# Kernel optimization log

Hardware: AMD Instinct MI355X
Metric: run time of the kernel (lower is better)

## Reference

```python
import jax, jax.numpy as jnp
import numpy as np


def _quant(x):
    # Per-tensor dynamic uint8 quantization to produce LUT row/col indices.
    # (The CUDA kernel's exact requant scheme is not in the source; this is the
    # assumed scheme: scale so max |x| -> 255, round, clip to [0,255].)
    s = 255.0 / jnp.maximum(jnp.max(jnp.abs(x)), jnp.float32(1e-6))
    return jnp.clip(jnp.round(x * s), 0, 255).astype(jnp.int32)


def _lut_conv(x, w, b, lut):
    # CustomAnyConv2d: stride=1, padding=(2,2), kernel 5x5.
    O, Cin, kh, kw = w.shape
    # im2col patches: (B, Cin*kh*kw, H, W), feature ordering matches w.reshape(O, -1)
    patches = jax.lax.conv_general_dilated_patches(
        x, (kh, kw), (1, 1), ((2, 2), (2, 2)))
    B, K, H, W = patches.shape
    pi = _quant(patches).reshape(B, K, H * W)            # (B,K,P)
    wi = _quant(w.reshape(O, K))                          # (O,K)
    vals = lut[pi[:, None, :, :], wi[None, :, :, None]]   # (B,O,K,P) gather
    out = vals.sum(axis=2).reshape(B, O, H, W)            # accumulate LUT products
    return out + b[None, :, None, None]


def _lut_dense(x, w, b, lut):
    # CustomAnyDense: out[h, o] = sum_k LUT[x[h,k], w[o,k]] + b[o]
    xi = _quant(x)                                        # (B,K)
    wi = _quant(w)                                        # (O,K)
    vals = lut[xi[:, None, :], wi[None, :, :]]            # (B,O,K)
    return vals.sum(axis=2) + b


def _maxpool2(x, pad=0):
    return jax.lax.reduce_window(
        x, -jnp.inf, jax.lax.max,
        (1, 1, 2, 2), (1, 1, 2, 2),
        ((0, 0), (0, 0), (pad, pad), (pad, pad)))


def setup_inputs() -> dict:
    key = jax.random.key(0)
    ks = jax.random.split(key, 11)
    B = 32
    x = jax.random.uniform(ks[0], (B, 1, 28, 28), jnp.float32)
    ij = np.arange(256)
    # Approximate-multiplier LUT: high byte of exact 8x8-bit product (uint8-valued).
    lut = jnp.asarray(((ij[:, None] * ij[None, :]) >> 8).astype(np.float32))
    return {
        "x": x,
        "lut": lut,
        "w1": jax.random.uniform(ks[1], (16, 1, 5, 5), jnp.float32),
        "b1": jax.random.normal(ks[2], (16,), jnp.float32) * 0.01,
        "w2": jax.random.uniform(ks[3], (32, 16, 5, 5), jnp.float32),
        "b2": jax.random.normal(ks[4], (32,), jnp.float32) * 0.01,
        "w3": jax.random.uniform(ks[5], (64, 32, 5, 5), jnp.float32),
        "b3": jax.random.normal(ks[6], (64,), jnp.float32) * 0.01,
        "fw1": jax.random.uniform(ks[7], (256, 1024), jnp.float32),
        "fb1": jax.random.normal(ks[8], (256,), jnp.float32) * 0.01,
        "fw2": jax.random.uniform(ks[9], (10, 256), jnp.float32),
        "fb2": jax.random.normal(ks[10], (10,), jnp.float32) * 0.01,
    }


def reference(x, lut, w1, b1, w2, b2, w3, b3, fw1, fb1, fw2, fb2):
    h = jax.nn.relu(_lut_conv(x, w1, b1, lut))
    h = _maxpool2(h)                     # (B,16,14,14)
    h = jax.nn.relu(_lut_conv(h, w2, b2, lut))
    h = _maxpool2(h)                     # (B,32,7,7)
    h = jax.nn.relu(_lut_conv(h, w3, b3, lut))
    h = _maxpool2(h, pad=1)              # (B,64,4,4)
    h = h.reshape(h.shape[0], -1)        # (B,1024)
    h = jax.nn.relu(_lut_dense(h, fw1, fb1, lut))
    h = _lut_dense(h, fw2, fb2, lut)     # (B,10)
    return jax.nn.log_softmax(h, axis=1)
```

## Files before the change

kernel.cpp:

```cpp
#include <hip/hip_runtime.h>
#include <math.h>

typedef unsigned int  u32;
typedef unsigned short u16;
typedef unsigned short u16x2 __attribute__((ext_vector_type(2)));

#define MAGIC 0x5A17D0E5u

#define O_FLAGS 256
#define O_QFW1  4096
#define O_QFW2  528384
#define O_A1    533504
#define O_A2    934912
#define O_A3    1135616
#define O_A4    1266688

__device__ __forceinline__ float blk_max(float v, float* red) {
  int t = threadIdx.x;
  __syncthreads();
  red[t] = v;
  __syncthreads();
#pragma unroll
  for (int s = 128; s > 0; s >>= 1) {
    if (t < s) red[t] = fmaxf(red[t], red[t + s]);
    __syncthreads();
  }
  return red[0];
}

__device__ __forceinline__ void amax_f(float* slot, float v) {
  atomicMax((int*)slot, (int)__float_as_uint(v));
}

__device__ __forceinline__ u16 quant1(float v, float s) {
  float q = rintf(v * s);
  q = fminf(fmaxf(q, 0.0f), 255.0f);
  return (u16)q;
}

__device__ __forceinline__ void mac_u32(u32& acc, u32 a, u32 w) {
  u16x2 av = __builtin_bit_cast(u16x2, a);
  u16x2 wv = __builtin_bit_cast(u16x2, w);
  u16x2 p  = av * wv;
  acc += (__builtin_bit_cast(u32, p) >> 8) & 0x00FF00FFu;
}
__device__ __forceinline__ void mac4(u32& acc, uint4 a, uint4 w) {
  mac_u32(acc, a.x, w.x); mac_u32(acc, a.y, w.y);
  mac_u32(acc, a.z, w.z); mac_u32(acc, a.w, w.w);
}

__device__ __forceinline__ float fmax4(float4 v) {
  return fmaxf(fmaxf(fabsf(v.x), fabsf(v.y)), fmaxf(fabsf(v.z), fabsf(v.w)));
}

__global__ __launch_bounds__(256) void k_conv1(
    const float* __restrict__ x, const float* __restrict__ w1, const float* __restrict__ b1,
    const float* __restrict__ w2, const float* __restrict__ w3,
    const float* __restrict__ fw1, const float* __restrict__ fw2,
    float* __restrict__ a1, float* wsf) {
  __shared__ unsigned char sx[32 * 32];
  __shared__ u16 sw[32];
  __shared__ float red[256];
  const int t = threadIdx.x, bid = blockIdx.x;

  if (bid >= 512) {
    int sb = bid - 512;
    const float* p; int n4, base, nb, slot;
    if (sb < 2)       { p = w2;  n4 = 3200;  base = sb;      nb = 2;  slot = 2; }
    else if (sb < 10) { p = w3;  n4 = 12800; base = sb - 2;  nb = 8;  slot = 3; }
    else if (sb < 58) { p = fw1; n4 = 65536; base = sb - 10; nb = 48; slot = 4; }
    else              { p = fw2; n4 = 640;   base = 0;       nb = 1;  slot = 5; }
    const float4* p4 = (const float4*)p;
    float m = 0.f;
    for (int i = base * 256 + t; i < n4; i += nb * 256) m = fmaxf(m, fmax4(p4[i]));
    m = blk_max(m, red);
    if (t == 0) amax_f(wsf + slot, m);
    return;
  }

  int b = bid >> 4, oc = bid & 15;
  float m = 0.f;
  const float4* x4 = (const float4*)x;
  for (int i = t; i < 6272; i += 256) m = fmaxf(m, fmax4(x4[i]));
  float xmax = blk_max(m, red);
  m = 0.f;
  if (t < 100) m = fmax4(((const float4*)w1)[t]);
  float w1max = blk_max(m, red);
  float s0 = 255.0f / fmaxf(xmax, 1e-6f);
  float sw1 = 255.0f / fmaxf(w1max, 1e-6f);

  u32* sxz = (u32*)sx;
  for (int i = t; i < 256; i += 256) sxz[i] = 0;
  __syncthreads();
  for (int i = t; i < 784; i += 256) {
    int y = i / 28, xx = i - y * 28;
    sx[(y + 2) * 32 + xx + 2] = (unsigned char)quant1(x[b * 784 + i], s0);
  }
  if (t < 25) sw[t] = quant1(w1[oc * 25 + t], sw1);
  __syncthreads();
  float lm = 0.f;
  if (t < 196) {
    int py = t / 14, px = t - py * 14;
    int best = -2147483647;
#pragma unroll
    for (int dy = 0; dy < 2; ++dy)
#pragma unroll
      for (int dx = 0; dx < 2; ++dx) {
        int cy = 2 * py + dy, cx = 2 * px + dx;
        int acc = 0;
#pragma unroll
        for (int kh = 0; kh < 5; ++kh) {
          const unsigned char* xp = sx + (cy + kh) * 32 + cx;
#pragma unroll
          for (int kw = 0; kw < 5; ++kw)
            acc += ((int)xp[kw] * (int)sw[kh * 5 + kw]) >> 8;
        }
        best = max(best, acc);
      }
    float v = fmaxf(0.f, (float)best + b1[oc]);
    a1[b * 3136 + t * 16 + oc] = v;
    lm = v;
  }
  lm = blk_max(lm, red);
  if (t == 0) amax_f(wsf + 6, lm);
}

__global__ __launch_bounds__(256) void k_conv2(
    const float* __restrict__ a1, const float* __restrict__ w2, const float* __restrict__ b2,
    const float* __restrict__ fw1, const float* __restrict__ fw2,
    float* __restrict__ a2, u16* __restrict__ qfw1, u16* __restrict__ qfw2, float* wsf) {
  __shared__ __align__(16) u16 sa[324 * 16];
  __shared__ __align__(16) u16 sw[800];
  __shared__ int sconv[196];
  __shared__ float red[256];
  const int t = threadIdx.x, bid = blockIdx.x;

  if (bid >= 512) {
    if (bid < 576) {
      float s = 255.0f / fmaxf(wsf[4], 1e-6f);
      for (int i = (bid - 512) * 256 + t; i < 262144; i += 64 * 256)
        qfw1[i] = quant1(fw1[i], s);
    } else {
      float s = 255.0f / fmaxf(wsf[5], 1e-6f);
      for (int i = t; i < 2560; i += 256) qfw2[i] = quant1(fw2[i], s);
    }
    return;
  }

  int b = bid >> 4, og = bid & 15;
  float s1 = 255.0f / fmaxf(wsf[6], 1e-6f);
  float sw2 = 255.0f / fmaxf(wsf[2], 1e-6f);
  u32* sz = (u32*)sa;
  for (int i = t; i < 2592; i += 256) sz[i] = 0;
  __syncthreads();
  for (int i = t; i < 3136; i += 256) {
    int px = i >> 4, c = i & 15;
    int y = px / 14, xx = px - y * 14;
    sa[((y + 2) * 18 + xx + 2) * 16 + c] = quant1(a1[b * 3136 + i], s1);
  }
  for (int i = t; i < 800; i += 256) {
    int ol = i / 400, r = i - ol * 400, c = r / 25, tp = r - c * 25;
    sw[ol * 400 + tp * 16 + c] = quant1(w2[(og * 2 + ol) * 400 + c * 25 + tp], sw2);
  }
  __syncthreads();
  int h = t & 1, pxb = t >> 1;
  float lm = 0.f;
  for (int ol = 0; ol < 2; ++ol) {
    int oc = og * 2 + ol;
    const uint4* wq = (const uint4*)(sw + ol * 400);
#pragma unroll
    for (int rep = 0; rep < 2; ++rep) {
      int px = pxb + rep * 128;
      if (px < 196) {
        int y = px / 14, xx = px - y * 14;
        u32 acc = 0;
#pragma unroll
        for (int kh = 0; kh < 5; ++kh)
#pragma unroll
          for (int kw = 0; kw < 5; ++kw) {
            int row = (y + kh) * 18 + (xx + kw);
            uint4 av = *(const uint4*)(sa + row * 16 + h * 8);
            mac4(acc, av, wq[(kh * 5 + kw) * 2 + h]);
          }
        int ai = (int)((acc & 0xFFFFu) + (acc >> 16));
        ai += __shfl_down(ai, 1, 2);
        if (h == 0) sconv[px] = ai;
      }
    }
    __syncthreads();
    if (t < 49) {
      int py = t / 7, px = t - py * 7;
      int mm = sconv[(2 * py) * 14 + 2 * px];
      mm = max(mm, sconv[(2 * py) * 14 + 2 * px + 1]);
      mm = max(mm, sconv[(2 * py + 1) * 14 + 2 * px]);
      mm = max(mm, sconv[(2 * py + 1) * 14 + 2 * px + 1]);
      float v = fmaxf(0.f, (float)mm + b2[oc]);
      a2[b * 1568 + t * 32 + oc] = v;
      lm = fmaxf(lm, v);
    }
    __syncthreads();
  }
  lm = blk_max(lm, red);
  if (t == 0) amax_f(wsf + 7, lm);
}

__global__ __launch_bounds__(256) void k_conv3(
    const float* __restrict__ a2, const float* __restrict__ w3, const float* __restrict__ b3,
    float* __restrict__ a3, float* wsf) {
  __shared__ __align__(16) u16 sa[121 * 40];
  __shared__ __align__(16) u16 sw[4 * 800];
  __shared__ float red[256];
  const int t = threadIdx.x, bid = blockIdx.x;
  int b = bid >> 4, og = bid & 15;
  float s2 = 255.0f / fmaxf(wsf[7], 1e-6f);
  float sw3 = 255.0f / fmaxf(wsf[3], 1e-6f);
  u32* sz = (u32*)sa;
  for (int i = t; i < 2420; i += 256) sz[i] = 0;
  __syncthreads();
  for (int i = t; i < 1568; i += 256) {
    int px = i >> 5, c = i & 31;
    int y = px / 7, xx = px - y * 7;
    sa[((y + 2) * 11 + xx + 2) * 40 + c] = quant1(a2[b * 1568 + i], s2);
  }
  for (int i = t; i < 3200; i += 256) {
    int ol = i / 800, r = i - ol * 800, c = r / 25, tp = r - c * 25;
    sw[ol * 800 + tp * 32 + c] = quant1(w3[(og * 4 + ol) * 800 + c * 25 + tp], sw3);
  }
  __syncthreads();
  int q = t & 3, pos = t >> 2;
  int dydx = pos & 3, r = pos >> 2;
  int py = r >> 2, px = r & 3;
  int cy = 2 * py - 1 + (dydx >> 1), cx = 2 * px - 1 + (dydx & 1);
  bool valid = (cy >= 0 && cy < 7 && cx >= 0 && cx < 7);
  float lm = 0.f;
  for (int ol = 0; ol < 4; ++ol) {
    int oc = og * 4 + ol;
    int ai = 0;
    if (valid) {
      u32 acc = 0;
#pragma unroll
      for (int kh = 0; kh < 5; ++kh)
#pragma unroll
        for (int kw = 0; kw < 5; ++kw) {
          int row = (cy + kh) * 11 + (cx + kw);
          uint4 av = *(const uint4*)(sa + row * 40 + q * 8);
          uint4 wv = *(const uint4*)(sw + ol * 800 + (kh * 5 + kw) * 32 + q * 8);
          mac4(acc, av, wv);
        }
      ai = (int)((acc & 0xFFFFu) + (acc >> 16));
    }
    ai += __shfl_down(ai, 2, 4);
    ai += __shfl_down(ai, 1, 4);
    int val = valid ? ai : -(1 << 30);
    int mm = max(val, __shfl_down(val, 4, 16));
    mm = max(mm, __shfl_down(mm, 8, 16));
    if ((t & 15) == 0) {
      float v = fmaxf(0.f, (float)mm + b3[oc]);
      a3[b * 1024 + oc * 16 + r] = v;
      lm = fmaxf(lm, v);
    }
  }
  lm = blk_max(lm, red);
  if (t == 0) amax_f(wsf + 8, lm);
}

__global__ __launch_bounds__(256) void k_dense12(
    const float* __restrict__ a3f, const u16* __restrict__ qfw1, const float* __restrict__ fb1,
    const u16* __restrict__ qfw2, const float* __restrict__ fb2,
    float* __restrict__ a4, float* __restrict__ out, float* wsf, u32* flags) {
  __shared__ union {
    struct { u16 sh[1024]; } p;
    struct { u16 sh2[32 * 264]; float zb[320]; } w;
  } sm;
  __shared__ float red[256];
  const int t = threadIdx.x, bid = blockIdx.x;

  if (bid < 512) {
    int b = bid >> 4, og = bid & 15;
    float s3 = 255.0f / fmaxf(wsf[8], 1e-6f);
    for (int i = t; i < 1024; i += 256)
      sm.p.sh[i] = quant1(a3f[b * 1024 + i], s3);
    __syncthreads();
    int ol = t >> 4, ks = t & 15;
    int o = og * 16 + ol;
    const uint4* wp = (const uint4*)(qfw1 + o * 1024);
    const uint4* hp = (const uint4*)sm.p.sh;
    u32 acc = 0;
#pragma unroll
    for (int j = 0; j < 8; ++j)
      mac4(acc, hp[j * 16 + ks], wp[j * 16 + ks]);
    int ai = (int)((acc & 0xFFFFu) + (acc >> 16));
#pragma unroll
    for (int d = 8; d > 0; d >>= 1)
      ai += __shfl_down(ai, d, 16);
    float lm = 0.f;
    if (ks == 0) {
      float v = fmaxf(0.f, (float)ai + fb1[o]);
      a4[b * 256 + o] = v;
      lm = v;
    }
    lm = blk_max(lm, red);
    if (t == 0) amax_f(wsf + 9, lm);
    __syncthreads();
    if (t == 0)
      __hip_atomic_store(&flags[bid], MAGIC, __ATOMIC_RELEASE, __HIP_MEMORY_SCOPE_AGENT);
    return;
  }

  {
    long it = 0;
    int ok = 0;
    do {
      u32 f1 = __hip_atomic_load(&flags[t],       __ATOMIC_RELAXED, __HIP_MEMORY_SCOPE_AGENT);
      u32 f2 = __hip_atomic_load(&flags[t + 256], __ATOMIC_RELAXED, __HIP_MEMORY_SCOPE_AGENT);
      ok = __syncthreads_and((f1 == MAGIC) && (f2 == MAGIC));
      if (!ok) __builtin_amdgcn_s_sleep(1);
    } while (!ok && ++it < 4000000);
    __threadfence();
  }
  float s4 = 255.0f / fmaxf(wsf[9], 1e-6f);
  for (int i = t; i < 8192; i += 256) {
    int b = i >> 8, k = i & 255;
    sm.w.sh2[b * 264 + k] = quant1(a4[i], s4);
  }
  __syncthreads();
  for (int task = t; task < 320; task += 256) {
    int b = task / 10, o = task - b * 10;
    const uint4* wp = (const uint4*)(qfw2 + o * 256);
    const uint4* hp = (const uint4*)(sm.w.sh2 + b * 264);
    u32 acc = 0;
#pragma unroll
    for (int j = 0; j < 32; ++j)
      mac4(acc, hp[j], wp[j]);
    sm.w.zb[task] = (float)((acc & 0xFFFFu) + (acc >> 16)) + fb2[o];
  }
  __syncthreads();
  for (int task = t; task < 320; task += 256) {
    int b = task / 10;
    const float* z = sm.w.zb + b * 10;
    float m = z[0];
#pragma unroll
    for (int j = 1; j < 10; ++j) m = fmaxf(m, z[j]);
    float se = 0.f;
#pragma unroll
    for (int j = 0; j < 10; ++j) se += expf(z[j] - m);
    out[task] = sm.w.zb[task] - (m + logf(se));
  }
}

extern "C" void kernel_launch(void* const* d_in, const int* in_sizes, int n_in,
                              void* d_out, int out_size, void* d_ws, size_t ws_size,
                              hipStream_t stream) {
  const float* x   = (const float*)d_in[0];
  const float* w1  = (const float*)d_in[2];
  const float* b1  = (const float*)d_in[3];
  const float* w2  = (const float*)d_in[4];
  const float* b2  = (const float*)d_in[5];
  const float* w3  = (const float*)d_in[6];
  const float* b3  = (const float*)d_in[7];
  const float* fw1 = (const float*)d_in[8];
  const float* fb1 = (const float*)d_in[9];
  const float* fw2 = (const float*)d_in[10];
  const float* fb2 = (const float*)d_in[11];
  float* out = (float*)d_out;
  unsigned char* ws8 = (unsigned char*)d_ws;
  float* wsf = (float*)d_ws;
  u32* flags = (u32*)(ws8 + O_FLAGS);
  u16* QFW1 = (u16*)(ws8 + O_QFW1);
  u16* QFW2 = (u16*)(ws8 + O_QFW2);
  float* A1 = (float*)(ws8 + O_A1);
  float* A2 = (float*)(ws8 + O_A2);
  float* A3 = (float*)(ws8 + O_A3);
  float* A4 = (float*)(ws8 + O_A4);

  k_conv1  <<<571, 256, 0, stream>>>(x, w1, b1, w2, w3, fw1, fw2, A1, wsf);
  k_conv2  <<<577, 256, 0, stream>>>(A1, w2, b2, fw1, fw2, A2, QFW1, QFW2, wsf);
  k_conv3  <<<512, 256, 0, stream>>>(A2, w3, b3, A3, wsf);
  k_dense12<<<513, 256, 0, stream>>>(A3, QFW1, fb1, QFW2, fb2, A4, out, wsf, flags);
}
```

Measured before the change: 148.3 us.

## Split x-max into flag-signalled blocks, fuse fw1/fw2 quantization into dense kernel

```diff
diff --git a/kernel.cpp b/kernel.cpp
--- a/kernel.cpp
+++ b/kernel.cpp
@@ -7,13 +7,12 @@
 
 #define MAGIC 0x5A17D0E5u
 
-#define O_FLAGS 256
-#define O_QFW1  4096
-#define O_QFW2  528384
-#define O_A1    533504
-#define O_A2    934912
-#define O_A3    1135616
-#define O_A4    1266688
+#define O_XFLAGS 256
+#define O_FLAGS  1024
+#define O_A1     4096
+#define O_A2     405504
+#define O_A3     606208
+#define O_A4     737280
 
 __device__ __forceinline__ float blk_max(float v, float* red) {
   int t = threadIdx.x;
@@ -53,18 +52,31 @@
   return fmaxf(fmaxf(fabsf(v.x), fabsf(v.y)), fmaxf(fabsf(v.z), fabsf(v.w)));
 }
 
-__global__ __launch_bounds__(256) void k_conv1(
+__global__ __launch_bounds__(256, 2) void k_conv1(
     const float* __restrict__ x, const float* __restrict__ w1, const float* __restrict__ b1,
     const float* __restrict__ w2, const float* __restrict__ w3,
     const float* __restrict__ fw1, const float* __restrict__ fw2,
-    float* __restrict__ a1, float* wsf) {
-  __shared__ unsigned char sx[32 * 32];
-  __shared__ u16 sw[32];
+    float* __restrict__ a1, float* wsf, u32* xflags) {
+  __shared__ float sxf[1024];
+  __shared__ unsigned char sx[1024];
+  __shared__ u16 sw[64];
   __shared__ float red[256];
   const int t = threadIdx.x, bid = blockIdx.x;
 
-  if (bid >= 512) {
-    int sb = bid - 512;
+  if (bid >= 256) {
+    int sb = bid - 256;
+    if (sb < 16) {
+      const float4* x4 = (const float4*)x;
+      float m = 0.f;
+      for (int i = sb * 256 + t; i < 6272; i += 16 * 256) m = fmaxf(m, fmax4(x4[i]));
+      m = blk_max(m, red);
+      if (t == 0) {
+        amax_f(wsf + 0, m);
+        __hip_atomic_store(&xflags[sb], MAGIC, __ATOMIC_RELEASE, __HIP_MEMORY_SCOPE_AGENT);
+      }
+      return;
+    }
+    sb -= 16;
     const float* p; int n4, base, nb, slot;
     if (sb < 2)       { p = w2;  n4 = 3200;  base = sb;      nb = 2;  slot = 2; }
     else if (sb < 10) { p = w3;  n4 = 12800; base = sb - 2;  nb = 8;  slot = 3; }
@@ -78,48 +90,57 @@
     return;
   }
 
-  int b = bid >> 4, oc = bid & 15;
+  int b = bid >> 3, op = bid & 7;
   float m = 0.f;
-  const float4* x4 = (const float4*)x;
-  for (int i = t; i < 6272; i += 256) m = fmaxf(m, fmax4(x4[i]));
-  float xmax = blk_max(m, red);
-  m = 0.f;
   if (t < 100) m = fmax4(((const float4*)w1)[t]);
   float w1max = blk_max(m, red);
-  float s0 = 255.0f / fmaxf(xmax, 1e-6f);
-  float sw1 = 255.0f / fmaxf(w1max, 1e-6f);
-
-  u32* sxz = (u32*)sx;
-  for (int i = t; i < 256; i += 256) sxz[i] = 0;
+  float sw1s = 255.0f / fmaxf(w1max, 1e-6f);
+  for (int i = t; i < 1024; i += 256) sxf[i] = 0.f;
   __syncthreads();
   for (int i = t; i < 784; i += 256) {
     int y = i / 28, xx = i - y * 28;
-    sx[(y + 2) * 32 + xx + 2] = (unsigned char)quant1(x[b * 784 + i], s0);
-  }
-  if (t < 25) sw[t] = quant1(w1[oc * 25 + t], sw1);
+    sxf[(y + 2) * 32 + xx + 2] = x[b * 784 + i];
+  }
+  if (t < 50) sw[t] = quant1(w1[op * 50 + t], sw1s);
+  {
+    int it = 0, ok = 0;
+    do {
+      u32 f = (t < 16) ? __hip_atomic_load(&xflags[t], __ATOMIC_RELAXED, __HIP_MEMORY_SCOPE_AGENT)
+                       : MAGIC;
+      ok = __syncthreads_and(f == MAGIC);
+      if (!ok) __builtin_amdgcn_s_sleep(1);
+    } while (!ok && ++it < 2000000);
+    __threadfence();
+  }
+  float s0 = 255.0f / fmaxf(wsf[0], 1e-6f);
+  for (int i = t; i < 1024; i += 256) sx[i] = (unsigned char)quant1(sxf[i], s0);
   __syncthreads();
   float lm = 0.f;
   if (t < 196) {
     int py = t / 14, px = t - py * 14;
-    int best = -2147483647;
-#pragma unroll
-    for (int dy = 0; dy < 2; ++dy)
-#pragma unroll
-      for (int dx = 0; dx < 2; ++dx) {
-        int cy = 2 * py + dy, cx = 2 * px + dx;
-        int acc = 0;
-#pragma unroll
-        for (int kh = 0; kh < 5; ++kh) {
-          const unsigned char* xp = sx + (cy + kh) * 32 + cx;
-#pragma unroll
-          for (int kw = 0; kw < 5; ++kw)
-            acc += ((int)xp[kw] * (int)sw[kh * 5 + kw]) >> 8;
+#pragma unroll
+    for (int ol = 0; ol < 2; ++ol) {
+      int oc = op * 2 + ol;
+      int best = -2147483647;
+#pragma unroll
+      for (int dy = 0; dy < 2; ++dy)
+#pragma unroll
+        for (int dx = 0; dx < 2; ++dx) {
+          int cy = 2 * py + dy, cx = 2 * px + dx;
+          int acc = 0;
+#pragma unroll
+          for (int kh = 0; kh < 5; ++kh) {
+            const unsigned char* xp = sx + (cy + kh) * 32 + cx;
+#pragma unroll
+            for (int kw = 0; kw < 5; ++kw)
+              acc += ((int)xp[kw] * (int)sw[ol * 25 + kh * 5 + kw]) >> 8;
+          }
+          best = max(best, acc);
         }
-        best = max(best, acc);
-      }
-    float v = fmaxf(0.f, (float)best + b1[oc]);
-    a1[b * 3136 + t * 16 + oc] = v;
-    lm = v;
+      float v = fmaxf(0.f, (float)best + b1[oc]);
+      a1[b * 3136 + t * 16 + oc] = v;
+      lm = fmaxf(lm, v);
+    }
   }
   lm = blk_max(lm, red);
   if (t == 0) amax_f(wsf + 6, lm);
@@ -127,26 +148,12 @@
 
 __global__ __launch_bounds__(256) void k_conv2(
     const float* __restrict__ a1, const float* __restrict__ w2, const float* __restrict__ b2,
-    const float* __restrict__ fw1, const float* __restrict__ fw2,
-    float* __restrict__ a2, u16* __restrict__ qfw1, u16* __restrict__ qfw2, float* wsf) {
+    float* __restrict__ a2, float* wsf) {
   __shared__ __align__(16) u16 sa[324 * 16];
   __shared__ __align__(16) u16 sw[800];
   __shared__ int sconv[196];
   __shared__ float red[256];
   const int t = threadIdx.x, bid = blockIdx.x;
-
-  if (bid >= 512) {
-    if (bid < 576) {
-      float s = 255.0f / fmaxf(wsf[4], 1e-6f);
-      for (int i = (bid - 512) * 256 + t; i < 262144; i += 64 * 256)
-        qfw1[i] = quant1(fw1[i], s);
-    } else {
-      float s = 255.0f / fmaxf(wsf[5], 1e-6f);
-      for (int i = t; i < 2560; i += 256) qfw2[i] = quant1(fw2[i], s);
-    }
-    return;
-  }
-
   int b = bid >> 4, og = bid & 15;
   float s1 = 255.0f / fmaxf(wsf[6], 1e-6f);
   float sw2 = 255.0f / fmaxf(wsf[2], 1e-6f);
@@ -265,12 +272,12 @@
 }
 
 __global__ __launch_bounds__(256) void k_dense12(
-    const float* __restrict__ a3f, const u16* __restrict__ qfw1, const float* __restrict__ fb1,
-    const u16* __restrict__ qfw2, const float* __restrict__ fb2,
+    const float* __restrict__ a3f, const float* __restrict__ fw1, const float* __restrict__ fb1,
+    const float* __restrict__ fw2, const float* __restrict__ fb2,
     float* __restrict__ a4, float* __restrict__ out, float* wsf, u32* flags) {
   __shared__ union {
     struct { u16 sh[1024]; } p;
-    struct { u16 sh2[32 * 264]; float zb[320]; } w;
+    struct { u16 sh2[32 * 264]; u16 qw[2560]; float zb[320]; } w;
   } sm;
   __shared__ float red[256];
   const int t = threadIdx.x, bid = blockIdx.x;
@@ -278,17 +285,26 @@
   if (bid < 512) {
     int b = bid >> 4, og = bid & 15;
     float s3 = 255.0f / fmaxf(wsf[8], 1e-6f);
+    float sws = 255.0f / fmaxf(wsf[4], 1e-6f);
     for (int i = t; i < 1024; i += 256)
       sm.p.sh[i] = quant1(a3f[b * 1024 + i], s3);
     __syncthreads();
     int ol = t >> 4, ks = t & 15;
     int o = og * 16 + ol;
-    const uint4* wp = (const uint4*)(qfw1 + o * 1024);
+    const float4* wf = (const float4*)(fw1 + o * 1024);
     const uint4* hp = (const uint4*)sm.p.sh;
     u32 acc = 0;
 #pragma unroll
-    for (int j = 0; j < 8; ++j)
-      mac4(acc, hp[j * 16 + ks], wp[j * 16 + ks]);
+    for (int j = 0; j < 8; ++j) {
+      int e = j * 16 + ks;
+      float4 f0 = wf[e * 2], f1 = wf[e * 2 + 1];
+      uint4 wv;
+      wv.x = (u32)quant1(f0.x, sws) | ((u32)quant1(f0.y, sws) << 16);
+      wv.y = (u32)quant1(f0.z, sws) | ((u32)quant1(f0.w, sws) << 16);
+      wv.z = (u32)quant1(f1.x, sws) | ((u32)quant1(f1.y, sws) << 16);
+      wv.w = (u32)quant1(f1.z, sws) | ((u32)quant1(f1.w, sws) << 16);
+      mac4(acc, hp[e], wv);
+    }
     int ai = (int)((acc & 0xFFFFu) + (acc >> 16));
 #pragma unroll
     for (int d = 8; d > 0; d >>= 1)
@@ -319,14 +335,16 @@
     __threadfence();
   }
   float s4 = 255.0f / fmaxf(wsf[9], 1e-6f);
+  float s5 = 255.0f / fmaxf(wsf[5], 1e-6f);
   for (int i = t; i < 8192; i += 256) {
     int b = i >> 8, k = i & 255;
     sm.w.sh2[b * 264 + k] = quant1(a4[i], s4);
   }
+  for (int i = t; i < 2560; i += 256) sm.w.qw[i] = quant1(fw2[i], s5);
   __syncthreads();
   for (int task = t; task < 320; task += 256) {
     int b = task / 10, o = task - b * 10;
-    const uint4* wp = (const uint4*)(qfw2 + o * 256);
+    const uint4* wp = (const uint4*)(sm.w.qw + o * 256);
     const uint4* hp = (const uint4*)(sm.w.sh2 + b * 264);
     u32 acc = 0;
 #pragma unroll
@@ -365,16 +383,15 @@
   float* out = (float*)d_out;
   unsigned char* ws8 = (unsigned char*)d_ws;
   float* wsf = (float*)d_ws;
-  u32* flags = (u32*)(ws8 + O_FLAGS);
-  u16* QFW1 = (u16*)(ws8 + O_QFW1);
-  u16* QFW2 = (u16*)(ws8 + O_QFW2);
+  u32* xflags = (u32*)(ws8 + O_XFLAGS);
+  u32* flags  = (u32*)(ws8 + O_FLAGS);
   float* A1 = (float*)(ws8 + O_A1);
   float* A2 = (float*)(ws8 + O_A2);
   float* A3 = (float*)(ws8 + O_A3);
   float* A4 = (float*)(ws8 + O_A4);
 
-  k_conv1  <<<571, 256, 0, stream>>>(x, w1, b1, w2, w3, fw1, fw2, A1, wsf);
-  k_conv2  <<<577, 256, 0, stream>>>(A1, w2, b2, fw1, fw2, A2, QFW1, QFW2, wsf);
+  k_conv1  <<<331, 256, 0, stream>>>(x, w1, b1, w2, w3, fw1, fw2, A1, wsf, xflags);
+  k_conv2  <<<512, 256, 0, stream>>>(A1, w2, b2, A2, wsf);
   k_conv3  <<<512, 256, 0, stream>>>(A2, w3, b3, A3, wsf);
-  k_dense12<<<513, 256, 0, stream>>>(A3, QFW1, fb1, QFW2, fb2, A4, out, wsf, flags);
-}
+  k_dense12<<<513, 256, 0, stream>>>(A3, fw1, fb1, fw2, fb2, A4, out, wsf, flags);
+}
```

Result: slower. 158.5 us (+6.9%).
